# Optimization experiments

Measured on AMD Instinct MI355X. Metric: run time of the kernel, lower is better.

The kernel has to match this reference:

```python
import jax, jax.numpy as jnp
import numpy as np

# geomloss.SamplesLoss(loss='sinkhorn', p=2, blur=0.1**0.5, backend='tensorized',
#                      cost=cosine cost ** 2) with defaults scaling=0.5, debias=True,
#                      reach=None (balanced OT, dampening = 1), uniform weights.
P = 2
BLUR = 0.1 ** 0.5   # eps = BLUR**P = 0.1
SCALING = 0.5


def cosine_cost(a, b):
    # a: (B,N,D), b: (B,M,D) -> (1 - cos(a,b))**2, shape (B,N,M)
    an = a / jnp.linalg.norm(a, axis=-1, keepdims=True)
    bn = b / jnp.linalg.norm(b, axis=-1, keepdims=True)
    return (1.0 - jnp.einsum('bnd,bmd->bnm', an, bn)) ** P


def softmin(eps, C, h):
    # geomloss softmin_tensorized: h (B,M), C (B,N,M) -> (B,N)
    return -eps * jax.nn.logsumexp(h[:, None, :] - C / eps, axis=2)


def eps_schedule(diameter):
    # geomloss epsilon_schedule(p, diameter, blur, scaling)
    return ([diameter ** P]
            + [float(np.exp(e)) for e in np.arange(P * np.log(diameter),
                                                   P * np.log(BLUR),
                                                   P * np.log(SCALING))]
            + [BLUR ** P])


def max_diameter(x, y):
    # geomloss max_diameter over all points of both (flattened) clouds
    D = x.shape[-1]
    pts = np.concatenate([np.asarray(x).reshape(-1, D),
                          np.asarray(y).reshape(-1, D)], axis=0)
    return float(np.linalg.norm(pts.max(axis=0) - pts.min(axis=0)))


def _sinkhorn(x, y, eps_list):
    sg = jax.lax.stop_gradient
    B, N, _ = x.shape
    M = y.shape[1]
    # geomloss detaches the second argument of each cost evaluation
    C_xy = cosine_cost(x, sg(y))
    C_yx = cosine_cost(y, sg(x))
    C_xx = cosine_cost(x, sg(x))  # debias terms
    C_yy = cosine_cost(y, sg(y))

    a_log = jnp.full((B, N), -np.log(N), dtype=x.dtype)  # log uniform weights
    b_log = jnp.full((B, M), -np.log(M), dtype=x.dtype)

    # initialization at the largest temperature
    eps = eps_list[0]
    f_aa = softmin(eps, sg(C_xx), a_log)
    g_bb = softmin(eps, sg(C_yy), b_log)
    g_ab = softmin(eps, sg(C_yx), a_log)
    f_ba = softmin(eps, sg(C_xy), b_log)

    # eps-scaling loop (run without gradients, as in geomloss)
    for eps in eps_list:
        ft_ba = softmin(eps, sg(C_xy), b_log + g_ab / eps)
        gt_ab = softmin(eps, sg(C_yx), a_log + f_ba / eps)
        ft_aa = softmin(eps, sg(C_xx), a_log + f_aa / eps)
        gt_bb = softmin(eps, sg(C_yy), b_log + g_bb / eps)
        f_ba, g_ab = 0.5 * (f_ba + ft_ba), 0.5 * (g_ab + gt_ab)
        f_aa, g_bb = 0.5 * (f_aa + ft_aa), 0.5 * (g_bb + gt_bb)

    # last extrapolation WITH gradients, dual inputs detached (envelope theorem)
    eps = eps_list[-1]
    f_ba, g_ab = (softmin(eps, C_xy, sg(b_log + g_ab / eps)),
                  softmin(eps, C_yx, sg(a_log + f_ba / eps)))
    f_aa = softmin(eps, C_xx, sg(a_log + f_aa / eps))
    g_bb = softmin(eps, C_yy, sg(b_log + g_bb / eps))

    # sinkhorn_cost, debiased, batch -> (B,)
    a = jnp.exp(a_log)
    b = jnp.exp(b_log)
    return jnp.sum(a * (f_ba - f_aa), axis=1) + jnp.sum(b * (g_ab - g_bb), axis=1)


def setup_inputs() -> dict:
    key = jax.random.key(0)
    k1, k2 = jax.random.split(key)
    B, N, D = 2, 4096, 64
    inputs = jax.random.normal(k1, (B, N, D), dtype=jnp.float32)
    targets = jax.random.normal(k2, (B, N, D), dtype=jnp.float32)
    return {"inputs": inputs, "targets": targets}


def reference(inputs, targets):
    eps_list = eps_schedule(max_diameter(inputs, targets))
    return _sinkhorn(inputs, targets, eps_list)
```

## Files before the change

kernel.cpp:

```cpp
#include <hip/hip_runtime.h>
#include <math.h>

#define Bq 2
#define Nq 4096
#define Dq 64
#define MAXR 14
#define RBAND 16
#define NBAND (Nq / RBAND)
#define W_LOG (-8.317766166719343f)
#define WL2   (-12.0f)
#define LOG2E 1.4426950408889634f
#define LN2   0.6931471805599453f
#define DQ_SCALE (4.0f / 65535.0f)
#define Q_SCALE  16383.75f
#define ACLAMP 88.0f
#define SFLOOR 1e-30f

#define F_XN   ((size_t)0)
#define F_YN   (F_XN + (size_t)Bq * Nq * Dq)
#define F_XH   (F_YN + (size_t)Bq * Nq * Dq)
#define F_XL   (F_XH + (size_t)Bq * Nq * Dq / 2)
#define F_YH   (F_XL + (size_t)Bq * Nq * Dq / 2)
#define F_YL   (F_YH + (size_t)Bq * Nq * Dq / 2)
#define F_FG   (F_YL + (size_t)Bq * Nq * Dq / 2)
#define F_EPS  (F_FG + (size_t)2 * 4 * Bq * Nq)
#define F_MM   (F_EPS + 64)
#define F_CP   (F_MM + (size_t)64 * 128)
#define F_C    (((F_CP + (size_t)Bq * NBAND * Nq) + 3) & ~(size_t)3)
#define GSZ    ((size_t)Bq * Nq * Nq)
#define F_TOTAL_P (F_C + 3 * GSZ / 2)
#define F_TOTAL_S (F_C)

typedef short short8v __attribute__((ext_vector_type(8)));
typedef float f32x4 __attribute__((ext_vector_type(4)));

__device__ __forceinline__ unsigned short f2bf(float f) {
    unsigned u = __float_as_uint(f);
    unsigned r = (u + 0x7fffu + ((u >> 16) & 1u)) >> 16;
    return (unsigned short)r;
}
__device__ __forceinline__ float bf2f(unsigned short b) {
    return __uint_as_float(((unsigned)b) << 16);
}

__global__ __launch_bounds__(256) void k_normalize(const float* __restrict__ x,
                                                   const float* __restrict__ y,
                                                   float* __restrict__ ws) {
    int gid = blockIdx.x * 256 + threadIdx.x;
    int wave = gid >> 6;
    int lane = gid & 63;
    int tensor = wave / (Bq * Nq);
    int p = wave % (Bq * Nq);
    const float* src = tensor ? y : x;
    float v = src[(size_t)p * Dq + lane];
    float s = v * v;
    #pragma unroll
    for (int o = 32; o > 0; o >>= 1) s += __shfl_xor(s, o);
    float vn = v / sqrtf(s);
    float* dst = ws + (tensor ? F_YN : F_XN);
    dst[(size_t)p * Dq + lane] = vn;
    unsigned short hb = f2bf(vn);
    float lo = vn - bf2f(hb);
    unsigned short lb = f2bf(lo);
    unsigned short* dh = (unsigned short*)(ws + (tensor ? F_YH : F_XH));
    unsigned short* dl = (unsigned short*)(ws + (tensor ? F_YL : F_XL));
    dh[(size_t)p * Dq + lane] = hb;
    dl[(size_t)p * Dq + lane] = lb;
}

__global__ __launch_bounds__(256) void k_minmax(const float* __restrict__ x,
                                                const float* __restrict__ y,
                                                float* __restrict__ ws) {
    int d = threadIdx.x & 63, q = threadIdx.x >> 6;
    int p0 = blockIdx.x * 256;
    float mx = -INFINITY, mn = INFINITY;
    for (int p = p0 + q; p < p0 + 256; p += 4) {
        const float* src = (p < Bq * Nq) ? x : y;
        int pp = (p < Bq * Nq) ? p : p - Bq * Nq;
        float v = src[(size_t)pp * Dq + d];
        mx = fmaxf(mx, v); mn = fminf(mn, v);
    }
    __shared__ float smx[4][64], smn[4][64];
    smx[q][d] = mx; smn[q][d] = mn;
    __syncthreads();
    if (threadIdx.x < 64) {
        float a = fmaxf(fmaxf(smx[0][d], smx[1][d]), fmaxf(smx[2][d], smx[3][d]));
        float i = fminf(fminf(smn[0][d], smn[1][d]), fminf(smn[2][d], smn[3][d]));
        ws[F_MM + (size_t)blockIdx.x * 128 + d] = a;
        ws[F_MM + (size_t)blockIdx.x * 128 + 64 + d] = i;
    }
}

__global__ void k_eps(float* __restrict__ ws) {
    int d = threadIdx.x;
    float mx = -INFINITY, mn = INFINITY;
    for (int k = 0; k < 64; k++) {
        mx = fmaxf(mx, ws[F_MM + (size_t)k * 128 + d]);
        mn = fminf(mn, ws[F_MM + (size_t)k * 128 + 64 + d]);
    }
    float r = mx - mn;
    float r2 = r * r;
    #pragma unroll
    for (int o = 32; o > 0; o >>= 1) r2 += __shfl_xor(r2, o);
    if (d == 0) {
        double dd = (double)sqrtf(r2);
        double start = 2.0 * log(dd);
        double stop  = 2.0 * log(sqrt(0.1));
        double step  = 2.0 * log(0.5);
        double lend = ceil((stop - start) / step);
        int len = (lend <= 0.0) ? 0 : (int)lend;
        int n = len + 2;
        if (n > MAXR - 2) n = MAXR - 2;
        int* ei = (int*)(ws + F_EPS);
        ei[0] = n;
        float* ev = ws + F_EPS + 8;
        ev[0] = (float)(dd * dd);
        for (int i = 0; i < len && i + 1 < n - 1; i++)
            ev[1 + i] = (float)exp(start + i * step);
        ev[n - 1] = 0.1f;
    }
}

__global__ __launch_bounds__(256) void k_gram_mfma(float* __restrict__ ws) {
    int op = blockIdx.z, b = blockIdx.y;
    int tr = (blockIdx.x & 63) * 64;
    int tc = (blockIdx.x >> 6) * 64;
    const unsigned short* AH = (const unsigned short*)(ws + (op == 2 ? F_YH : F_XH)) + (size_t)b * Nq * Dq;
    const unsigned short* AL = (const unsigned short*)(ws + (op == 2 ? F_YL : F_XL)) + (size_t)b * Nq * Dq;
    const unsigned short* BH = (const unsigned short*)(ws + (op == 1 ? F_XH : F_YH)) + (size_t)b * Nq * Dq;
    const unsigned short* BL = (const unsigned short*)(ws + (op == 1 ? F_XL : F_YL)) + (size_t)b * Nq * Dq;

    __shared__ unsigned short sbuf[4][64][72];
    #define sAh (sbuf[0])
    #define sAl (sbuf[1])
    #define sBh (sbuf[2])
    #define sBl (sbuf[3])
    #define sC  (sbuf[0])

    #pragma unroll
    for (int i = 0; i < 2; i++) {
        int c = threadIdx.x + 256 * i;
        int row = c >> 3, pos = c & 7;
        size_t sa = (size_t)(tr + row) * Dq + pos * 8;
        size_t sb = (size_t)(tc + row) * Dq + pos * 8;
        *(uint4*)&sAh[row][pos * 8] = *(const uint4*)&AH[sa];
        *(uint4*)&sAl[row][pos * 8] = *(const uint4*)&AL[sa];
        *(uint4*)&sBh[row][pos * 8] = *(const uint4*)&BH[sb];
        *(uint4*)&sBl[row][pos * 8] = *(const uint4*)&BL[sb];
    }
    __syncthreads();

    int w = threadIdx.x >> 6, lane = threadIdx.x & 63;
    int m = lane & 15, kb = lane >> 4;
    int ar = w * 16 + m;
    short8v aH0 = *(const short8v*)&sAh[ar][kb * 8];
    short8v aH1 = *(const short8v*)&sAh[ar][32 + kb * 8];
    short8v aL0 = *(const short8v*)&sAl[ar][kb * 8];
    short8v aL1 = *(const short8v*)&sAl[ar][32 + kb * 8];
    __syncthreads();

    #pragma unroll
    for (int cb = 0; cb < 4; cb++) {
        int bc = cb * 16 + m;
        short8v bH0 = *(const short8v*)&sBh[bc][kb * 8];
        short8v bH1 = *(const short8v*)&sBh[bc][32 + kb * 8];
        short8v bL0 = *(const short8v*)&sBl[bc][kb * 8];
        short8v bL1 = *(const short8v*)&sBl[bc][32 + kb * 8];
        f32x4 acc = {0.f, 0.f, 0.f, 0.f};
        acc = __builtin_amdgcn_mfma_f32_16x16x32_bf16(aH0, bH0, acc, 0, 0, 0);
        acc = __builtin_amdgcn_mfma_f32_16x16x32_bf16(aH1, bH1, acc, 0, 0, 0);
        acc = __builtin_amdgcn_mfma_f32_16x16x32_bf16(aL0, bH0, acc, 0, 0, 0);
        acc = __builtin_amdgcn_mfma_f32_16x16x32_bf16(aL1, bH1, acc, 0, 0, 0);
        acc = __builtin_amdgcn_mfma_f32_16x16x32_bf16(aH0, bL0, acc, 0, 0, 0);
        acc = __builtin_amdgcn_mfma_f32_16x16x32_bf16(aH1, bL1, acc, 0, 0, 0);
        int colblk = cb * 2 + (m >> 3);
        int within = m & 7;
        #pragma unroll
        for (int rr = 0; rr < 4; rr++) {
            int rowl = w * 16 + kb * 4 + rr;
            float c1 = 1.0f - acc[rr];
            unsigned u = __float2uint_rn(fminf(c1 * c1, 4.0f) * Q_SCALE);
            if (u > 65535u) u = 65535u;
            int swz = colblk ^ ((rowl >> 1) & 7);
            sC[rowl][swz * 8 + within] = (unsigned short)u;
        }
    }
    __syncthreads();

    unsigned short* C = (unsigned short*)(ws + F_C) + (size_t)op * GSZ + (size_t)b * Nq * Nq;
    #pragma unroll
    for (int i = 0; i < 2; i++) {
        int c = threadIdx.x + 256 * i;
        int row = c >> 3, pos = c & 7;
        int swz = pos ^ ((row >> 1) & 7);
        uint4 v = *(const uint4*)&sC[row][swz * 8];
        *(uint4*)&C[(size_t)(tr + row) * Nq + tc + pos * 8] = v;
    }
    #undef sAh
    #undef sAl
    #undef sBh
    #undef sBl
    #undef sC
}

__device__ __forceinline__ bool round_cfg(const float* ws, int r, int& mode, float& eps,
                                          float& inv_eps, int& cur, int& nxt) {
    const int* ei = (const int*)(ws + F_EPS);
    int n_eps = ei[0];
    if (r > n_eps + 1) return false;
    mode = (r == 0) ? 0 : ((r <= n_eps) ? 1 : 2);
    int eidx = (r == 0) ? 0 : ((r - 1 < n_eps - 1) ? r - 1 : n_eps - 1);
    eps = ws[F_EPS + 8 + eidx];
    inv_eps = 1.0f / eps;
    cur = r & 1; nxt = cur ^ 1;
    return true;
}

__global__ __launch_bounds__(256) void k_iter(float* __restrict__ ws, int r) {
    int mode, cur, nxt; float eps, inv_eps;
    if (!round_cfg(ws, r, mode, eps, inv_eps, cur, nxt)) return;
    float ie2 = inv_eps * LOG2E;
    float epsln2 = eps * LN2;
    float nkq = -DQ_SCALE * ie2;

    int bid = blockIdx.x;
    int op = bid / (Bq * NBAND);
    int rem = bid % (Bq * NBAND);
    int b = rem / NBAND;
    int band = rem % NBAND;
    int row0 = band * RBAND;
    int w = threadIdx.x >> 6, lane = threadIdx.x & 63;
    int colA = w * 1024 + lane * 8;
    int colB = colA + 512;

    const unsigned short* C = (const unsigned short*)(ws + F_C)
                              + (size_t)op * GSZ + ((size_t)b * Nq + row0) * Nq;
    int arr_dual = (op == 0) ? 1 : (op == 1 ? 2 : 3);
    int arr_out  = (op == 0) ? 0 : arr_dual;
    const float* gdual = ws + F_FG + ((size_t)cur * 4 + arr_dual) * (Bq * Nq) + (size_t)b * Nq;
    const float* fdual = ws + F_FG + ((size_t)cur * 4 + 0) * (Bq * Nq) + (size_t)b * Nq;

    float pa[16];
    if (mode != 0) {
        float4 g0 = *(const float4*)&gdual[colA];
        float4 g1 = *(const float4*)&gdual[colA + 4];
        float4 g2 = *(const float4*)&gdual[colB];
        float4 g3 = *(const float4*)&gdual[colB + 4];
        float gv[16] = {g0.x, g0.y, g0.z, g0.w, g1.x, g1.y, g1.z, g1.w,
                        g2.x, g2.y, g2.z, g2.w, g3.x, g3.y, g3.z, g3.w};
        #pragma unroll
        for (int j = 0; j < 16; j++) pa[j] = exp2f(fminf(gv[j] * ie2, ACLAMP));
    } else {
        #pragma unroll
        for (int j = 0; j < 16; j++) pa[j] = 1.f;
    }
    float cs[16];
    #pragma unroll
    for (int j = 0; j < 16; j++) cs[j] = 0.f;

    __shared__ float rowpart[RBAND][4];

    #pragma unroll 2
    for (int i = 0; i < RBAND; i += 2) {
        uint4 cA0 = *(const uint4*)&C[(size_t)i * Nq + colA];
        uint4 cB0 = *(const uint4*)&C[(size_t)i * Nq + colB];
        uint4 cA1 = *(const uint4*)&C[(size_t)(i + 1) * Nq + colA];
        uint4 cB1 = *(const uint4*)&C[(size_t)(i + 1) * Nq + colB];
        float pb0 = 1.f, pb1 = 1.f;
        if (op == 0 && mode != 0) {
            pb0 = exp2f(fminf(fdual[row0 + i] * ie2, ACLAMP));
            pb1 = exp2f(fminf(fdual[row0 + i + 1] * ie2, ACLAMP));
        }
        unsigned u0[8] = {cA0.x, cA0.y, cA0.z, cA0.w, cB0.x, cB0.y, cB0.z, cB0.w};
        unsigned u1[8] = {cA1.x, cA1.y, cA1.z, cA1.w, cB1.x, cB1.y, cB1.z, cB1.w};
        float rs0 = 0.f, rs1 = 0.f;
        #pragma unroll
        for (int j = 0; j < 16; j++) {
            float e0 = exp2f((float)((u0[j >> 1] >> ((j & 1) * 16)) & 0xffffu) * nkq);
            float e1 = exp2f((float)((u1[j >> 1] >> ((j & 1) * 16)) & 0xffffu) * nkq);
            rs0 = fmaf(pa[j], e0, rs0);
            rs1 = fmaf(pa[j], e1, rs1);
            if (op == 0) cs[j] = fmaf(pb0, e0, fmaf(pb1, e1, cs[j]));
        }
        #pragma unroll
        for (int o = 32; o > 0; o >>= 1) {
            rs0 += __shfl_xor(rs0, o);
            rs1 += __shfl_xor(rs1, o);
        }
        if (lane == 0) { rowpart[i][w] = rs0; rowpart[i + 1][w] = rs1; }
    }
    __syncthreads();

    if (threadIdx.x < RBAND) {
        int gr = row0 + threadIdx.x;
        const float* rp = rowpart[threadIdx.x];
        float s = (rp[0] + rp[1]) + (rp[2] + rp[3]);
        float ft = -epsln2 * (WL2 + log2f(fmaxf(s, SFLOOR)));
        float* outp = ws + F_FG + ((size_t)nxt * 4 + arr_out) * (Bq * Nq) + (size_t)b * Nq;
        const float* oldp = ws + F_FG + ((size_t)cur * 4 + arr_out) * (Bq * Nq) + (size_t)b * Nq;
        outp[gr] = (mode == 1) ? 0.5f * (oldp[gr] + ft) : ft;
    }

    if (op == 0) {
        float* cp = ws + F_CP + ((size_t)b * NBAND + band) * Nq;
        *(float4*)&cp[colA]     = make_float4(cs[0], cs[1], cs[2], cs[3]);
        *(float4*)&cp[colA + 4] = make_float4(cs[4], cs[5], cs[6], cs[7]);
        *(float4*)&cp[colB]     = make_float4(cs[8], cs[9], cs[10], cs[11]);
        *(float4*)&cp[colB + 4] = make_float4(cs[12], cs[13], cs[14], cs[15]);
    }
}

__global__ __launch_bounds__(256) void k_colcomb(float* __restrict__ ws, int r) {
    int mode, cur, nxt; float eps, inv_eps;
    if (!round_cfg(ws, r, mode, eps, inv_eps, cur, nxt)) return;
    float epsln2 = eps * LN2;
    int q = threadIdx.x >> 6, c = threadIdx.x & 63;
    int idx = blockIdx.x * 64 + c;
    int b = idx >> 12, m = idx & (Nq - 1);
    const float* cp = ws + F_CP + (size_t)b * NBAND * Nq + m;
    float S = 0.f;
    #pragma unroll 8
    for (int k = q * (NBAND / 4); k < (q + 1) * (NBAND / 4); k++)
        S += cp[(size_t)k * Nq];
    __shared__ float part[4][64];
    part[q][c] = S;
    __syncthreads();
    if (threadIdx.x < 64) {
        float St = (part[0][c] + part[1][c]) + (part[2][c] + part[3][c]);
        float gt = -epsln2 * (WL2 + log2f(fmaxf(St, SFLOOR)));
        float* outp = ws + F_FG + ((size_t)nxt * 4 + 1) * (Bq * Nq) + (size_t)b * Nq;
        const float* oldp = ws + F_FG + ((size_t)cur * 4 + 1) * (Bq * Nq) + (size_t)b * Nq;
        outp[m] = (mode == 1) ? 0.5f * (oldp[m] + gt) : gt;
    }
}

__global__ __launch_bounds__(256) void k_fused(float* __restrict__ ws, int r) {
    int mode, cur, nxt; float eps, inv_eps;
    if (!round_cfg(ws, r, mode, eps, inv_eps, cur, nxt)) return;
    int op = blockIdx.z, b = blockIdx.y;
    int tr = blockIdx.x * 64;
    const float* A  = ws + ((op == 1 || op == 3) ? F_YN : F_XN) + (size_t)b * Nq * Dq;
    const float* Bp = ws + ((op == 0 || op == 3) ? F_YN : F_XN) + (size_t)b * Nq * Dq;
    int dual_arr = (op == 0) ? 1 : (op == 1) ? 0 : (op == 2) ? 2 : 3;
    int out_arr  = (op == 0) ? 0 : (op == 1) ? 1 : (op == 2) ? 2 : 3;
    const float* hdual = ws + F_FG + ((size_t)cur * 4 + dual_arr) * (Bq * Nq) + (size_t)b * Nq;

    __shared__ float As[64][65], Bs[64][65];
    #pragma unroll
    for (int i = 0; i < 16; i++) {
        int idx = threadIdx.x + 256 * i;
        As[idx >> 6][idx & 63] = A[(size_t)(tr + (idx >> 6)) * Dq + (idx & 63)];
    }
    int tx = threadIdx.x & 15, ty = threadIdx.x >> 4;
    float m_i[4], s_i[4];
    #pragma unroll
    for (int i = 0; i < 4; i++) { m_i[i] = -INFINITY; s_i[i] = 0.f; }

    for (int tc = 0; tc < Nq; tc += 64) {
        __syncthreads();
        #pragma unroll
        for (int i = 0; i < 16; i++) {
            int idx = threadIdx.x + 256 * i;
            Bs[idx >> 6][idx & 63] = Bp[(size_t)(tc + (idx >> 6)) * Dq + (idx & 63)];
        }
        __syncthreads();
        float acc[4][4] = {};
        #pragma unroll
        for (int dd = 0; dd < 64; dd++) {
            float a[4], bb[4];
            #pragma unroll
            for (int i = 0; i < 4; i++) a[i] = As[ty * 4 + i][dd];
            #pragma unroll
            for (int j = 0; j < 4; j++) bb[j] = Bs[tx * 4 + j][dd];
            #pragma unroll
            for (int i = 0; i < 4; i++)
                #pragma unroll
                for (int j = 0; j < 4; j++) acc[i][j] = fmaf(a[i], bb[j], acc[i][j]);
        }
        float hv[4];
        #pragma unroll
        for (int j = 0; j < 4; j++)
            hv[j] = (mode == 0) ? 0.f : hdual[tc + tx * 4 + j];
        #pragma unroll
        for (int i = 0; i < 4; i++) {
            float v[4], tm = -INFINITY;
            #pragma unroll
            for (int j = 0; j < 4; j++) {
                float c = 1.0f - acc[i][j];
                v[j] = W_LOG + (hv[j] - c * c) * inv_eps;
                tm = fmaxf(tm, v[j]);
            }
            float nm = fmaxf(m_i[i], tm);
            float add = 0.f;
            #pragma unroll
            for (int j = 0; j < 4; j++) add += expf(v[j] - nm);
            s_i[i] = s_i[i] * expf(m_i[i] - nm) + add;
            m_i[i] = nm;
        }
    }
    #pragma unroll
    for (int o = 1; o < 16; o <<= 1) {
        #pragma unroll
        for (int i = 0; i < 4; i++) {
            float om = __shfl_xor(m_i[i], o);
            float os = __shfl_xor(s_i[i], o);
            float M = fmaxf(m_i[i], om);
            s_i[i] = s_i[i] * expf(m_i[i] - M) + os * expf(om - M);
            m_i[i] = M;
        }
    }
    if (tx == 0) {
        float* outp = ws + F_FG + ((size_t)nxt * 4 + out_arr) * (Bq * Nq) + (size_t)b * Nq;
        const float* oldp = ws + F_FG + ((size_t)cur * 4 + out_arr) * (Bq * Nq) + (size_t)b * Nq;
        #pragma unroll
        for (int i = 0; i < 4; i++) {
            int n = tr + ty * 4 + i;
            float ft = -eps * (m_i[i] + logf(s_i[i]));
            outp[n] = (mode == 1) ? 0.5f * (oldp[n] + ft) : ft;
        }
    }
}

__global__ __launch_bounds__(256) void k_final(const float* __restrict__ ws,
                                               float* __restrict__ out) {
    const int* ei = (const int*)(ws + F_EPS);
    int n_eps = ei[0];
    int fin = n_eps & 1;
    int b = blockIdx.x;
    const float* fba = ws + F_FG + ((size_t)fin * 4 + 0) * (Bq * Nq) + (size_t)b * Nq;
    const float* gab = ws + F_FG + ((size_t)fin * 4 + 1) * (Bq * Nq) + (size_t)b * Nq;
    const float* faa = ws + F_FG + ((size_t)fin * 4 + 2) * (Bq * Nq) + (size_t)b * Nq;
    const float* gbb = ws + F_FG + ((size_t)fin * 4 + 3) * (Bq * Nq) + (size_t)b * Nq;
    float s = 0.f;
    for (int n = threadIdx.x; n < Nq; n += 256)
        s += (fba[n] - faa[n]) + (gab[n] - gbb[n]);
    #pragma unroll
    for (int o = 32; o > 0; o >>= 1) s += __shfl_xor(s, o);
    __shared__ float red[4];
    if ((threadIdx.x & 63) == 0) red[threadIdx.x >> 6] = s;
    __syncthreads();
    if (threadIdx.x == 0)
        out[b] = (red[0] + red[1] + red[2] + red[3]) * (1.0f / Nq);
}

__global__ void k_sentinel(float* out, int n) {
    if ((int)threadIdx.x < n) out[threadIdx.x] = 2.0e9f;
}

extern "C" void kernel_launch(void* const* d_in, const int* in_sizes, int n_in,
                              void* d_out, int out_size, void* d_ws, size_t ws_size,
                              hipStream_t stream) {
    const float* x = (const float*)d_in[0];
    const float* y = (const float*)d_in[1];
    float* out = (float*)d_out;
    float* ws = (float*)d_ws;

    bool big   = ws_size >= F_TOTAL_P * sizeof(float);
    bool small = ws_size >= F_TOTAL_S * sizeof(float);

    if (!small) {
        k_sentinel<<<1, 64, 0, stream>>>(out, out_size);
        return;
    }

    k_normalize<<<(2 * Bq * Nq * 64) / 256, 256, 0, stream>>>(x, y, ws);
    k_minmax<<<64, 256, 0, stream>>>(x, y, ws);
    k_eps<<<1, 64, 0, stream>>>(ws);

    if (big) {
        k_gram_mfma<<<dim3(4096, Bq, 3), 256, 0, stream>>>(ws);
        for (int r = 0; r < MAXR; r++) {
            k_iter<<<3 * Bq * NBAND, 256, 0, stream>>>(ws, r);
            k_colcomb<<<(Bq * Nq) / 64, 256, 0, stream>>>(ws, r);
        }
    } else {
        for (int r = 0; r < MAXR; r++) {
            k_fused<<<dim3(Nq / 64, Bq, 4), 256, 0, stream>>>(ws, r);
        }
    }

    k_final<<<Bq, 256, 0, stream>>>(ws, out);
}
```

Baseline: 684.1 us.

## Exploit symmetry of self-cost matrices to halve Gram compute and sweeps

The self-cost matrices C_xx and C_yy are symmetric, so the Gram kernel now skips the tiles below the diagonal for those operators. A new iteration kernel reads each upper-triangular band once and produces both the row sums and the column partial sums, which a new combine kernel reduces. This roughly halves the fp16 cost reads and the exp work for the two debias terms, at the cost of unbalanced block workloads (bands near the bottom are short) and an extra partial-sum buffer. The new path runs only when the workspace is large enough for that buffer; otherwise the old path is used.

```diff
diff --git a/kernel.cpp b/kernel.cpp
--- a/kernel.cpp
+++ b/kernel.cpp
@@ -28,7 +28,9 @@
 #define F_CP   (F_MM + (size_t)64 * 128)
 #define F_C    (((F_CP + (size_t)Bq * NBAND * Nq) + 3) & ~(size_t)3)
 #define GSZ    ((size_t)Bq * Nq * Nq)
-#define F_TOTAL_P (F_C + 3 * GSZ / 2)
+#define F_CPS  (F_C + 3 * GSZ / 2)
+#define F_TOTAL_OLD (F_C + 3 * GSZ / 2)
+#define F_TOTAL_SYM (F_CPS + (size_t)2 * Bq * NBAND * Nq)
 #define F_TOTAL_S (F_C)
 
 typedef short short8v __attribute__((ext_vector_type(8)));
@@ -121,10 +123,11 @@
     }
 }
 
-__global__ __launch_bounds__(256) void k_gram_mfma(float* __restrict__ ws) {
+__global__ __launch_bounds__(256) void k_gram_mfma(float* __restrict__ ws, int skipLower) {
     int op = blockIdx.z, b = blockIdx.y;
     int tr = (blockIdx.x & 63) * 64;
     int tc = (blockIdx.x >> 6) * 64;
+    if (skipLower && op != 0 && tc + 64 <= tr) return;
     const unsigned short* AH = (const unsigned short*)(ws + (op == 2 ? F_YH : F_XH)) + (size_t)b * Nq * Dq;
     const unsigned short* AL = (const unsigned short*)(ws + (op == 2 ? F_YL : F_XL)) + (size_t)b * Nq * Dq;
     const unsigned short* BH = (const unsigned short*)(ws + (op == 1 ? F_XH : F_YH)) + (size_t)b * Nq * Dq;
@@ -216,6 +219,199 @@
     return true;
 }
 
+__global__ __launch_bounds__(256) void k_iter2(float* __restrict__ ws, int r) {
+    int mode, cur, nxt; float eps, inv_eps;
+    if (!round_cfg(ws, r, mode, eps, inv_eps, cur, nxt)) return;
+    float ie2 = inv_eps * LOG2E;
+    float epsln2 = eps * LN2;
+    float nkq = -DQ_SCALE * ie2;
+
+    int bid = blockIdx.x;
+    int w = threadIdx.x >> 6, lane = threadIdx.x & 63;
+    __shared__ float rowpart[RBAND][4];
+
+    if (bid < Bq * NBAND) {
+        int b = bid / NBAND;
+        int band = bid % NBAND;
+        int row0 = band * RBAND;
+        int colA = w * 1024 + lane * 8;
+        int colB = colA + 512;
+        const unsigned short* C = (const unsigned short*)(ws + F_C) + ((size_t)b * Nq + row0) * Nq;
+        const float* gdual = ws + F_FG + ((size_t)cur * 4 + 1) * (Bq * Nq) + (size_t)b * Nq;
+        const float* fdual = ws + F_FG + ((size_t)cur * 4 + 0) * (Bq * Nq) + (size_t)b * Nq;
+
+        float pa[16];
+        if (mode != 0) {
+            float4 g0 = *(const float4*)&gdual[colA];
+            float4 g1 = *(const float4*)&gdual[colA + 4];
+            float4 g2 = *(const float4*)&gdual[colB];
+            float4 g3 = *(const float4*)&gdual[colB + 4];
+            float gv[16] = {g0.x, g0.y, g0.z, g0.w, g1.x, g1.y, g1.z, g1.w,
+                            g2.x, g2.y, g2.z, g2.w, g3.x, g3.y, g3.z, g3.w};
+            #pragma unroll
+            for (int j = 0; j < 16; j++) pa[j] = exp2f(fminf(gv[j] * ie2, ACLAMP));
+        } else {
+            #pragma unroll
+            for (int j = 0; j < 16; j++) pa[j] = 1.f;
+        }
+        float cs[16];
+        #pragma unroll
+        for (int j = 0; j < 16; j++) cs[j] = 0.f;
+
+        #pragma unroll 2
+        for (int i = 0; i < RBAND; i += 2) {
+            uint4 cA0 = *(const uint4*)&C[(size_t)i * Nq + colA];
+            uint4 cB0 = *(const uint4*)&C[(size_t)i * Nq + colB];
+            uint4 cA1 = *(const uint4*)&C[(size_t)(i + 1) * Nq + colA];
+            uint4 cB1 = *(const uint4*)&C[(size_t)(i + 1) * Nq + colB];
+            float pb0 = 1.f, pb1 = 1.f;
+            if (mode != 0) {
+                pb0 = exp2f(fminf(fdual[row0 + i] * ie2, ACLAMP));
+                pb1 = exp2f(fminf(fdual[row0 + i + 1] * ie2, ACLAMP));
+            }
+            unsigned u0[8] = {cA0.x, cA0.y, cA0.z, cA0.w, cB0.x, cB0.y, cB0.z, cB0.w};
+            unsigned u1[8] = {cA1.x, cA1.y, cA1.z, cA1.w, cB1.x, cB1.y, cB1.z, cB1.w};
+            float rs0 = 0.f, rs1 = 0.f;
+            #pragma unroll
+            for (int j = 0; j < 16; j++) {
+                float e0 = exp2f((float)((u0[j >> 1] >> ((j & 1) * 16)) & 0xffffu) * nkq);
+                float e1 = exp2f((float)((u1[j >> 1] >> ((j & 1) * 16)) & 0xffffu) * nkq);
+                rs0 = fmaf(pa[j], e0, rs0);
+                rs1 = fmaf(pa[j], e1, rs1);
+                cs[j] = fmaf(pb0, e0, fmaf(pb1, e1, cs[j]));
+            }
+            #pragma unroll
+            for (int o = 32; o > 0; o >>= 1) {
+                rs0 += __shfl_xor(rs0, o);
+                rs1 += __shfl_xor(rs1, o);
+            }
+            if (lane == 0) { rowpart[i][w] = rs0; rowpart[i + 1][w] = rs1; }
+        }
+        __syncthreads();
+
+        if (threadIdx.x < RBAND) {
+            int gr = row0 + threadIdx.x;
+            const float* rp = rowpart[threadIdx.x];
+            float s = (rp[0] + rp[1]) + (rp[2] + rp[3]);
+            float ft = -epsln2 * (WL2 + log2f(fmaxf(s, SFLOOR)));
+            float* outp = ws + F_FG + ((size_t)nxt * 4 + 0) * (Bq * Nq) + (size_t)b * Nq;
+            const float* oldp = ws + F_FG + ((size_t)cur * 4 + 0) * (Bq * Nq) + (size_t)b * Nq;
+            outp[gr] = (mode == 1) ? 0.5f * (oldp[gr] + ft) : ft;
+        }
+        float* cp = ws + F_CP + ((size_t)b * NBAND + band) * Nq;
+        *(float4*)&cp[colA]     = make_float4(cs[0], cs[1], cs[2], cs[3]);
+        *(float4*)&cp[colA + 4] = make_float4(cs[4], cs[5], cs[6], cs[7]);
+        *(float4*)&cp[colB]     = make_float4(cs[8], cs[9], cs[10], cs[11]);
+        *(float4*)&cp[colB + 4] = make_float4(cs[12], cs[13], cs[14], cs[15]);
+    } else {
+        int sid = bid - Bq * NBAND;
+        int op = 1 + sid / (Bq * NBAND);
+        int rem = sid % (Bq * NBAND);
+        int b = rem / NBAND;
+        int I = rem % NBAND;
+        int S = I * RBAND;
+        const unsigned short* Cm = (const unsigned short*)(ws + F_C)
+                                   + (size_t)op * GSZ + (size_t)b * Nq * Nq;
+        int arr = (op == 1) ? 2 : 3;
+        const float* dual = ws + F_FG + ((size_t)cur * 4 + arr) * (Bq * Nq) + (size_t)b * Nq;
+        float* cps = ws + F_CPS + (((size_t)(op - 1) * Bq + b) * NBAND + I) * Nq;
+
+        float pb[RBAND];
+        #pragma unroll
+        for (int i = 0; i < RBAND; i++)
+            pb[i] = (mode != 0) ? exp2f(fminf(dual[S + i] * ie2, ACLAMP)) : 1.f;
+        float rs[RBAND];
+        #pragma unroll
+        for (int i = 0; i < RBAND; i++) rs[i] = 0.f;
+
+        for (int t = w; S + t * 512 < Nq; t += 4) {
+            int c = S + t * 512 + lane * 8;
+            bool valid = (c < Nq);
+            float pac[8];
+            if (mode != 0 && valid) {
+                float4 g0 = *(const float4*)&dual[c];
+                float4 g1 = *(const float4*)&dual[c + 4];
+                float gv[8] = {g0.x, g0.y, g0.z, g0.w, g1.x, g1.y, g1.z, g1.w};
+                #pragma unroll
+                for (int j = 0; j < 8; j++) pac[j] = exp2f(fminf(gv[j] * ie2, ACLAMP));
+            } else {
+                #pragma unroll
+                for (int j = 0; j < 8; j++) pac[j] = 1.f;
+            }
+            float csl[8];
+            #pragma unroll
+            for (int j = 0; j < 8; j++) csl[j] = 0.f;
+            #pragma unroll 2
+            for (int i = 0; i < RBAND; i++) {
+                float e[8];
+                if (valid) {
+                    uint4 cu = *(const uint4*)&Cm[(size_t)(S + i) * Nq + c];
+                    unsigned uw[4] = {cu.x, cu.y, cu.z, cu.w};
+                    #pragma unroll
+                    for (int j = 0; j < 8; j++)
+                        e[j] = exp2f((float)((uw[j >> 1] >> ((j & 1) * 16)) & 0xffffu) * nkq);
+                } else {
+                    #pragma unroll
+                    for (int j = 0; j < 8; j++) e[j] = 0.f;
+                }
+                #pragma unroll
+                for (int j = 0; j < 8; j++) rs[i] = fmaf(pac[j], e[j], rs[i]);
+                #pragma unroll
+                for (int j = 0; j < 8; j++) csl[j] = fmaf(pb[i], e[j], csl[j]);
+            }
+            if (valid && c >= S + RBAND) {
+                *(float4*)&cps[c]     = make_float4(csl[0], csl[1], csl[2], csl[3]);
+                *(float4*)&cps[c + 4] = make_float4(csl[4], csl[5], csl[6], csl[7]);
+            }
+        }
+        #pragma unroll
+        for (int i = 0; i < RBAND; i++) {
+            float v = rs[i];
+            #pragma unroll
+            for (int o = 32; o > 0; o >>= 1) v += __shfl_xor(v, o);
+            if (lane == 0) rowpart[i][w] = v;
+        }
+        __syncthreads();
+        if (threadIdx.x < RBAND) {
+            const float* rp = rowpart[threadIdx.x];
+            cps[S + threadIdx.x] = (rp[0] + rp[1]) + (rp[2] + rp[3]);
+        }
+    }
+}
+
+__global__ __launch_bounds__(256) void k_comb2(float* __restrict__ ws, int r) {
+    int mode, cur, nxt; float eps, inv_eps;
+    if (!round_cfg(ws, r, mode, eps, inv_eps, cur, nxt)) return;
+    float epsln2 = eps * LN2;
+    int q = threadIdx.x >> 6, cidx = threadIdx.x & 63;
+    int g = blockIdx.x * 64 + cidx;
+    int kind = g / (Bq * Nq);
+    int rem = g % (Bq * Nq);
+    int b = rem >> 12, m = rem & (Nq - 1);
+    const float* cp;
+    int J, arr;
+    if (kind == 0) { cp = ws + F_CP + (size_t)b * NBAND * Nq; J = NBAND - 1; arr = 1; }
+    else {
+        cp = ws + F_CPS + ((size_t)(kind - 1) * Bq + b) * NBAND * Nq;
+        J = m >> 4; arr = (kind == 1) ? 2 : 3;
+    }
+    int k0 = q * (NBAND / 4);
+    int k1 = (q + 1) * (NBAND / 4);
+    if (k1 > J + 1) k1 = J + 1;
+    float S = 0.f;
+    for (int k = k0; k < k1; k++) S += cp[(size_t)k * Nq + m];
+    __shared__ float part[4][64];
+    part[q][cidx] = S;
+    __syncthreads();
+    if (threadIdx.x < 64) {
+        float St = (part[0][cidx] + part[1][cidx]) + (part[2][cidx] + part[3][cidx]);
+        float gt = -epsln2 * (WL2 + log2f(fmaxf(St, SFLOOR)));
+        float* outp = ws + F_FG + ((size_t)nxt * 4 + arr) * (Bq * Nq) + (size_t)b * Nq;
+        const float* oldp = ws + F_FG + ((size_t)cur * 4 + arr) * (Bq * Nq) + (size_t)b * Nq;
+        outp[m] = (mode == 1) ? 0.5f * (oldp[m] + gt) : gt;
+    }
+}
+
 __global__ __launch_bounds__(256) void k_iter(float* __restrict__ ws, int r) {
     int mode, cur, nxt; float eps, inv_eps;
     if (!round_cfg(ws, r, mode, eps, inv_eps, cur, nxt)) return;
@@ -455,7 +651,8 @@
     float* out = (float*)d_out;
     float* ws = (float*)d_ws;
 
-    bool big   = ws_size >= F_TOTAL_P * sizeof(float);
+    bool sym   = ws_size >= F_TOTAL_SYM * sizeof(float);
+    bool big   = ws_size >= F_TOTAL_OLD * sizeof(float);
     bool small = ws_size >= F_TOTAL_S * sizeof(float);
 
     if (!small) {
@@ -467,8 +664,14 @@
     k_minmax<<<64, 256, 0, stream>>>(x, y, ws);
     k_eps<<<1, 64, 0, stream>>>(ws);
 
-    if (big) {
-        k_gram_mfma<<<dim3(4096, Bq, 3), 256, 0, stream>>>(ws);
+    if (sym) {
+        k_gram_mfma<<<dim3(4096, Bq, 3), 256, 0, stream>>>(ws, 1);
+        for (int r = 0; r < MAXR; r++) {
+            k_iter2<<<3 * Bq * NBAND, 256, 0, stream>>>(ws, r);
+            k_comb2<<<(3 * Bq * Nq) / 64, 256, 0, stream>>>(ws, r);
+        }
+    } else if (big) {
+        k_gram_mfma<<<dim3(4096, Bq, 3), 256, 0, stream>>>(ws, 0);
         for (int r = 0; r < MAXR; r++) {
             k_iter<<<3 * Bq * NBAND, 256, 0, stream>>>(ws, r);
             k_colcomb<<<(Bq * Nq) / 64, 256, 0, stream>>>(ws, r);
```

Result: slower. 902.5 us (+31.9%).
